# Performance work log

Hardware: AMD Instinct MI355X
Metric: run time of the kernel (lower is better)

The kernel has to match this reference:

```python
import jax, jax.numpy as jnp
import numpy as np

S, I, H, FC, O = 16384, 64, 1024, 128, 1


def setup_inputs() -> dict:
    key = jax.random.key(0)
    ks = jax.random.split(key, 9)
    s_lstm = 1.0 / np.sqrt(H)
    return {
        "input_seq": jax.random.normal(ks[0], (S, I), jnp.float32),
        "W_ih": jax.random.uniform(ks[1], (4 * H, I), jnp.float32, -s_lstm, s_lstm),
        "W_hh": jax.random.uniform(ks[2], (4 * H, H), jnp.float32, -s_lstm, s_lstm),
        "b_ih": jax.random.uniform(ks[3], (4 * H,), jnp.float32, -s_lstm, s_lstm),
        "b_hh": jax.random.uniform(ks[4], (4 * H,), jnp.float32, -s_lstm, s_lstm),
        "fc1_w": jax.random.uniform(ks[5], (FC, H), jnp.float32, -s_lstm, s_lstm),
        "fc1_b": jax.random.uniform(ks[6], (FC,), jnp.float32, -s_lstm, s_lstm),
        "fc2_w": jax.random.uniform(ks[7], (O, FC), jnp.float32, -1.0 / np.sqrt(FC), 1.0 / np.sqrt(FC)),
        "fc2_b": jax.random.uniform(ks[8], (O,), jnp.float32, -1.0 / np.sqrt(FC), 1.0 / np.sqrt(FC)),
    }


def _lstm_scan(x, W_ih, W_hh, b_ih, b_hh):
    # PyTorch gate order: i, f, g, o. batch=1 collapsed; x: [S, I]
    xg = x @ W_ih.T + (b_ih + b_hh)  # precompute input-side gates: [S, 4H]

    def step(carry, xg_t):
        h, c = carry
        gates = xg_t + h @ W_hh.T
        i, f, g, o = jnp.split(gates, 4)
        i = jax.nn.sigmoid(i)
        f = jax.nn.sigmoid(f)
        g = jnp.tanh(g)
        o = jax.nn.sigmoid(o)
        c = f * c + i * g
        h = o * jnp.tanh(c)
        return (h, c), h

    h0 = jnp.zeros((H,), x.dtype)
    c0 = jnp.zeros((H,), x.dtype)
    _, hs = jax.lax.scan(step, (h0, c0), xg)
    return hs  # [S, H]


def reference(input_seq, W_ih, W_hh, b_ih, b_hh, fc1_w, fc1_b, fc2_w, fc2_b):
    hs = _lstm_scan(input_seq, W_ih, W_hh, b_ih, b_hh)       # [S, H]
    x = jax.nn.relu(hs)                                       # relu on LSTM outputs
    x = jax.nn.relu(x @ fc1_w.T + fc1_b)                      # [S, 128]
    x = x @ fc2_w.T + fc2_b                                   # [S, 1]
    return x[-1]                                              # [1]
```

## Files before the change

kernel.cpp:

```cpp
#include <hip/hip_runtime.h>
#include <hip/hip_fp16.h>


#define S_LEN 16384
#define I_DIM 64
#define H_DIM 1024
#define NBLK  64
#define NTHR  512

typedef _Float16 half2_t __attribute__((ext_vector_type(2)));

__device__ __forceinline__ float sigmoidf_(float x) { return 1.0f / (1.0f + __expf(-x)); }
__device__ __forceinline__ float tanh_fast(float x) { return 1.0f - 2.0f / (__expf(2.0f * x) + 1.0f); }
__device__ __forceinline__ unsigned pack2(float a, float b) {
    return (unsigned)__half_as_ushort(__float2half(a)) |
           ((unsigned)__half_as_ushort(__float2half(b)) << 16);
}

__global__ __launch_bounds__(NTHR, 2) void lstm_persistent(
    const float* __restrict__ xseq,
    const float* __restrict__ W_ih,
    const float* __restrict__ W_hh,
    const float* __restrict__ b_ih,
    const float* __restrict__ b_hh,
    unsigned* __restrict__ pairs)
{
    const int b   = blockIdx.x;
    const int tid = threadIdx.x;
    const int w   = tid >> 6;
    const int c   = tid & 63;

    __shared__ unsigned h_stage[H_DIM / 2];
    __shared__ float    x_stage[2][I_DIM];
    __shared__ float    gs[64];
    __shared__ float    bias_s[64];

    unsigned wreg[8][8];
    float    wi[8];
    #pragma unroll
    for (int r = 0; r < 8; ++r) {
        const int rr   = 8 * w + r;
        const int grow = (rr >> 4) * H_DIM + 16 * b + (rr & 15);
        const float4* base = (const float4*)(W_hh + (size_t)grow * H_DIM);
        #pragma unroll
        for (int s = 0; s < 4; ++s) {
            const float4 f = base[s * 64 + c];
            wreg[r][2 * s]     = pack2(f.x, f.y);
            wreg[r][2 * s + 1] = pack2(f.z, f.w);
        }
        wi[r] = W_ih[(size_t)grow * I_DIM + c];
    }
    #pragma unroll
    for (int r = 0; r < 8; ++r)
        asm volatile("" : "+v"(wreg[r][0]), "+v"(wreg[r][1]), "+v"(wreg[r][2]),
                          "+v"(wreg[r][3]), "+v"(wreg[r][4]), "+v"(wreg[r][5]),
                          "+v"(wreg[r][6]), "+v"(wreg[r][7]));

    if (tid < 64) {
        const int grow = (tid >> 4) * H_DIM + 16 * b + (tid & 15);
        bias_s[tid] = b_ih[grow] + b_hh[grow];
    }
    float cst = 0.0f;
    h_stage[tid] = 0u;
    if (tid < 16) ((float4*)x_stage[0])[tid] = ((const float4*)xseq)[tid];
    __syncthreads();

    for (int t = 0; t < S_LEN; ++t) {
        if (w == 7 && c < 16 && t + 1 < S_LEN)
            ((float4*)x_stage[(t + 1) & 1])[c] =
                ((const float4*)(xseq + (size_t)(t + 1) * I_DIM))[c];

        float acc[8] = {0.f, 0.f, 0.f, 0.f, 0.f, 0.f, 0.f, 0.f};
        #pragma unroll
        for (int s = 0; s < 4; ++s) {
            const uint2 hv = *(const uint2*)&h_stage[s * 128 + 2 * c];
            const half2_t ha = __builtin_bit_cast(half2_t, hv.x);
            const half2_t hb = __builtin_bit_cast(half2_t, hv.y);
            #pragma unroll
            for (int r = 0; r < 8; ++r) {
                acc[r] = __builtin_amdgcn_fdot2(__builtin_bit_cast(half2_t, wreg[r][2 * s]),     ha, acc[r], false);
                acc[r] = __builtin_amdgcn_fdot2(__builtin_bit_cast(half2_t, wreg[r][2 * s + 1]), hb, acc[r], false);
            }
        }
        {
            const float xv = x_stage[t & 1][c];
            #pragma unroll
            for (int r = 0; r < 8; ++r) acc[r] = fmaf(wi[r], xv, acc[r]);
        }
        #pragma unroll
        for (int r = 0; r < 8; ++r) {
            #pragma unroll
            for (int off = 32; off > 0; off >>= 1)
                acc[r] += __shfl_xor(acc[r], off, 64);
        }
        if (c == 0) {
            #pragma unroll
            for (int r = 0; r < 8; ++r) gs[8 * w + r] = acc[r];
        }
        __syncthreads();

        if (tid < 16) {
            const float pi  = gs[tid]      + bias_s[tid];
            const float pfg = gs[16 + tid] + bias_s[16 + tid];
            const float pg  = gs[32 + tid] + bias_s[32 + tid];
            const float po  = gs[48 + tid] + bias_s[48 + tid];
            const float ig = sigmoidf_(pi);
            const float fg = sigmoidf_(pfg);
            const float gg = tanh_fast(pg);
            const float og = sigmoidf_(po);
            cst = fg * cst + ig * gg;
            const float h = og * tanh_fast(cst);
            const unsigned pk = ((unsigned)(t + 1) << 16) |
                                (unsigned)__half_as_ushort(__float2half(h));
            __hip_atomic_store(&pairs[(size_t)(t & 1) * H_DIM + 16 * b + tid], pk,
                               __ATOMIC_RELAXED, __HIP_MEMORY_SCOPE_AGENT);
        }

        if (t == S_LEN - 1) break;

        {
            const unsigned long long* P =
                (const unsigned long long*)(pairs + (size_t)(t & 1) * H_DIM);
            const unsigned long long tag  = (unsigned long long)(unsigned)(t + 1);
            const unsigned long long expv = (tag << 48) | (tag << 16);
            unsigned long long v;
            for (;;) {
                v = __hip_atomic_load(P + tid, __ATOMIC_RELAXED, __HIP_MEMORY_SCOPE_AGENT);
                if ((v & 0xFFFF0000FFFF0000ull) == expv) break;
                __builtin_amdgcn_s_sleep(1);
            }
            h_stage[tid] = (unsigned)(v & 0xFFFFu) | (((unsigned)(v >> 32) & 0xFFFFu) << 16);
        }
        __syncthreads();
    }
}

__global__ __launch_bounds__(256) void fc_head(
    const unsigned* __restrict__ pairs,
    const float* __restrict__ fc1_w,
    const float* __restrict__ fc1_b,
    const float* __restrict__ fc2_w,
    const float* __restrict__ fc2_b,
    float* __restrict__ out)
{
    const int tid = threadIdx.x;
    __shared__ float4 hr4[H_DIM / 4];
    __shared__ float  partial[256];
    __shared__ float  r1[128];

    const uint4 pa = ((const uint4*)(pairs + H_DIM))[tid];
    float4 hv = make_float4(__half2float(__ushort_as_half((unsigned short)(pa.x & 0xFFFFu))),
                            __half2float(__ushort_as_half((unsigned short)(pa.y & 0xFFFFu))),
                            __half2float(__ushort_as_half((unsigned short)(pa.z & 0xFFFFu))),
                            __half2float(__ushort_as_half((unsigned short)(pa.w & 0xFFFFu))));
    hv.x = fmaxf(hv.x, 0.f); hv.y = fmaxf(hv.y, 0.f);
    hv.z = fmaxf(hv.z, 0.f); hv.w = fmaxf(hv.w, 0.f);
    hr4[tid] = hv;
    __syncthreads();

    const int row = tid & 127, half = tid >> 7;
    const float4* wrow = (const float4*)(fc1_w + (size_t)row * H_DIM) + half * 128;
    float a0 = 0.f, a1 = 0.f;
    #pragma unroll 4
    for (int i = 0; i < 128; i += 2) {
        const float4 w0 = wrow[i],     h0 = hr4[half * 128 + i];
        const float4 w1 = wrow[i + 1], h1 = hr4[half * 128 + i + 1];
        a0 += w0.x * h0.x + w0.y * h0.y + w0.z * h0.z + w0.w * h0.w;
        a1 += w1.x * h1.x + w1.y * h1.y + w1.z * h1.z + w1.w * h1.w;
    }
    partial[tid] = a0 + a1;
    __syncthreads();
    if (tid < 128) {
        const float s = partial[tid] + partial[tid + 128] + fc1_b[tid];
        r1[tid] = fmaxf(s, 0.f);
    }
    __syncthreads();
    if (tid < 64) {
        float v = r1[tid] * fc2_w[tid] + r1[tid + 64] * fc2_w[tid + 64];
        #pragma unroll
        for (int off = 32; off > 0; off >>= 1) v += __shfl_xor(v, off, 64);
        if (tid == 0) out[0] = v + fc2_b[0];
    }
}

extern "C" void kernel_launch(void* const* d_in, const int* in_sizes, int n_in,
                              void* d_out, int out_size, void* d_ws, size_t ws_size,
                              hipStream_t stream) {
    (void)in_sizes; (void)n_in; (void)out_size; (void)ws_size;
    const float* xseq  = (const float*)d_in[0];
    const float* W_ih  = (const float*)d_in[1];
    const float* W_hh  = (const float*)d_in[2];
    const float* b_ih  = (const float*)d_in[3];
    const float* b_hh  = (const float*)d_in[4];
    const float* fc1_w = (const float*)d_in[5];
    const float* fc1_b = (const float*)d_in[6];
    const float* fc2_w = (const float*)d_in[7];
    const float* fc2_b = (const float*)d_in[8];
    unsigned* pairs = (unsigned*)d_ws;

    lstm_persistent<<<NBLK, NTHR, 0, stream>>>(xseq, W_ih, W_hh, b_ih, b_hh, pairs);
    fc_head<<<1, 256, 0, stream>>>(pairs, fc1_w, fc1_b, fc2_w, fc2_b, (float*)d_out);
}
```

Baseline: 41.11 ms.

## Fuse gate activations into each wave and exchange packed half2 hidden pairs

Each wave now owns two hidden units across all four gates. Lane 0 of the wave applies the activations right after the shuffle reduction, which removes the shared-memory gate staging and one block barrier per step. Hidden state is published as 64-bit words holding a 32-bit step tag and a packed half2 value. Each block writes its own results straight into a double-buffered shared h_stage and skips polling for them. The W_hh half2 registers are now reloaded from global memory every timestep before the spin-wait, which adds a large amount of per-step memory traffic.

```diff
diff --git a/kernel.cpp b/kernel.cpp
--- a/kernel.cpp
+++ b/kernel.cpp
@@ -16,6 +16,7 @@
     return (unsigned)__half_as_ushort(__float2half(a)) |
            ((unsigned)__half_as_ushort(__float2half(b)) << 16);
 }
+__device__ __forceinline__ half2_t as_h2(unsigned u) { return __builtin_bit_cast(half2_t, u); }
 
 __global__ __launch_bounds__(NTHR, 2) void lstm_persistent(
     const float* __restrict__ xseq,
@@ -23,63 +24,55 @@
     const float* __restrict__ W_hh,
     const float* __restrict__ b_ih,
     const float* __restrict__ b_hh,
-    unsigned* __restrict__ pairs)
+    unsigned long long* __restrict__ pairs)
 {
     const int b   = blockIdx.x;
     const int tid = threadIdx.x;
     const int w   = tid >> 6;
     const int c   = tid & 63;
 
-    __shared__ unsigned h_stage[H_DIM / 2];
+    __shared__ unsigned h_stage[2][H_DIM / 2];
     __shared__ float    x_stage[2][I_DIM];
-    __shared__ float    gs[64];
-    __shared__ float    bias_s[64];
-
-    unsigned wreg[8][8];
-    float    wi[8];
+
+    const float* wbase[8];
+    float wi[8], bias[8];
     #pragma unroll
     for (int r = 0; r < 8; ++r) {
-        const int rr   = 8 * w + r;
-        const int grow = (rr >> 4) * H_DIM + 16 * b + (rr & 15);
-        const float4* base = (const float4*)(W_hh + (size_t)grow * H_DIM);
+        const int grow = (r >> 1) * H_DIM + 16 * b + 2 * w + (r & 1);
+        wbase[r] = W_hh + (size_t)grow * H_DIM;
+        wi[r]    = W_ih[(size_t)grow * I_DIM + c];
+        bias[r]  = b_ih[grow] + b_hh[grow];
+    }
+    float cst0 = 0.f, cst1 = 0.f;
+
+    h_stage[0][tid] = 0u;
+    if (tid < 16) ((float4*)x_stage[0])[tid] = ((const float4*)xseq)[tid];
+    float4 xcur = make_float4(0.f, 0.f, 0.f, 0.f);
+    if (w == 7 && c < 16) xcur = ((const float4*)(xseq + (size_t)1 * I_DIM))[c];
+
+    unsigned wreg[8][8];
+    #pragma unroll
+    for (int r = 0; r < 8; ++r) {
+        const float4* b4 = (const float4*)wbase[r];
         #pragma unroll
         for (int s = 0; s < 4; ++s) {
-            const float4 f = base[s * 64 + c];
+            const float4 f = b4[s * 64 + c];
             wreg[r][2 * s]     = pack2(f.x, f.y);
             wreg[r][2 * s + 1] = pack2(f.z, f.w);
         }
-        wi[r] = W_ih[(size_t)grow * I_DIM + c];
-    }
-    #pragma unroll
-    for (int r = 0; r < 8; ++r)
-        asm volatile("" : "+v"(wreg[r][0]), "+v"(wreg[r][1]), "+v"(wreg[r][2]),
-                          "+v"(wreg[r][3]), "+v"(wreg[r][4]), "+v"(wreg[r][5]),
-                          "+v"(wreg[r][6]), "+v"(wreg[r][7]));
-
-    if (tid < 64) {
-        const int grow = (tid >> 4) * H_DIM + 16 * b + (tid & 15);
-        bias_s[tid] = b_ih[grow] + b_hh[grow];
-    }
-    float cst = 0.0f;
-    h_stage[tid] = 0u;
-    if (tid < 16) ((float4*)x_stage[0])[tid] = ((const float4*)xseq)[tid];
+    }
     __syncthreads();
 
     for (int t = 0; t < S_LEN; ++t) {
-        if (w == 7 && c < 16 && t + 1 < S_LEN)
-            ((float4*)x_stage[(t + 1) & 1])[c] =
-                ((const float4*)(xseq + (size_t)(t + 1) * I_DIM))[c];
-
         float acc[8] = {0.f, 0.f, 0.f, 0.f, 0.f, 0.f, 0.f, 0.f};
         #pragma unroll
         for (int s = 0; s < 4; ++s) {
-            const uint2 hv = *(const uint2*)&h_stage[s * 128 + 2 * c];
-            const half2_t ha = __builtin_bit_cast(half2_t, hv.x);
-            const half2_t hb = __builtin_bit_cast(half2_t, hv.y);
+            const uint2 hv = *(const uint2*)&h_stage[t & 1][s * 128 + 2 * c];
+            const half2_t ha = as_h2(hv.x), hb = as_h2(hv.y);
             #pragma unroll
             for (int r = 0; r < 8; ++r) {
-                acc[r] = __builtin_amdgcn_fdot2(__builtin_bit_cast(half2_t, wreg[r][2 * s]),     ha, acc[r], false);
-                acc[r] = __builtin_amdgcn_fdot2(__builtin_bit_cast(half2_t, wreg[r][2 * s + 1]), hb, acc[r], false);
+                acc[r] = __builtin_amdgcn_fdot2(as_h2(wreg[r][2 * s]),     ha, acc[r], false);
+                acc[r] = __builtin_amdgcn_fdot2(as_h2(wreg[r][2 * s + 1]), hb, acc[r], false);
             }
         }
         {
@@ -93,50 +86,69 @@
             for (int off = 32; off > 0; off >>= 1)
                 acc[r] += __shfl_xor(acc[r], off, 64);
         }
+
         if (c == 0) {
-            #pragma unroll
-            for (int r = 0; r < 8; ++r) gs[8 * w + r] = acc[r];
-        }
-        __syncthreads();
-
-        if (tid < 16) {
-            const float pi  = gs[tid]      + bias_s[tid];
-            const float pfg = gs[16 + tid] + bias_s[16 + tid];
-            const float pg  = gs[32 + tid] + bias_s[32 + tid];
-            const float po  = gs[48 + tid] + bias_s[48 + tid];
-            const float ig = sigmoidf_(pi);
-            const float fg = sigmoidf_(pfg);
-            const float gg = tanh_fast(pg);
-            const float og = sigmoidf_(po);
-            cst = fg * cst + ig * gg;
-            const float h = og * tanh_fast(cst);
-            const unsigned pk = ((unsigned)(t + 1) << 16) |
-                                (unsigned)__half_as_ushort(__float2half(h));
-            __hip_atomic_store(&pairs[(size_t)(t & 1) * H_DIM + 16 * b + tid], pk,
+            const float i0 = sigmoidf_(acc[0] + bias[0]);
+            const float f0 = sigmoidf_(acc[2] + bias[2]);
+            const float g0 = tanh_fast(acc[4] + bias[4]);
+            const float o0 = sigmoidf_(acc[6] + bias[6]);
+            cst0 = f0 * cst0 + i0 * g0;
+            const float h0 = o0 * tanh_fast(cst0);
+            const float i1 = sigmoidf_(acc[1] + bias[1]);
+            const float f1 = sigmoidf_(acc[3] + bias[3]);
+            const float g1 = tanh_fast(acc[5] + bias[5]);
+            const float o1 = sigmoidf_(acc[7] + bias[7]);
+            cst1 = f1 * cst1 + i1 * g1;
+            const float h1 = o1 * tanh_fast(cst1);
+            const unsigned lo = pack2(h0, h1);
+            const unsigned long long pk =
+                ((unsigned long long)(unsigned)(t + 1) << 32) | (unsigned long long)lo;
+            __hip_atomic_store(&pairs[(size_t)(t & 1) * (H_DIM / 2) + 8 * b + w], pk,
                                __ATOMIC_RELAXED, __HIP_MEMORY_SCOPE_AGENT);
+            h_stage[(t + 1) & 1][8 * b + w] = lo;
+        }
+
+        if (w == 7 && c < 16) {
+            if (t + 1 < S_LEN) ((float4*)x_stage[(t + 1) & 1])[c] = xcur;
+            const int tn = (t + 2 < S_LEN) ? t + 2 : S_LEN - 1;
+            xcur = ((const float4*)(xseq + (size_t)tn * I_DIM))[c];
         }
 
         if (t == S_LEN - 1) break;
 
-        {
-            const unsigned long long* P =
-                (const unsigned long long*)(pairs + (size_t)(t & 1) * H_DIM);
-            const unsigned long long tag  = (unsigned long long)(unsigned)(t + 1);
-            const unsigned long long expv = (tag << 48) | (tag << 16);
+        #pragma unroll
+        for (int r = 0; r < 8; ++r) {
+            const float4* b4 = (const float4*)wbase[r];
+            #pragma unroll
+            for (int s = 0; s < 4; ++s) {
+                const float4 f = b4[s * 64 + c];
+                wreg[r][2 * s]     = pack2(f.x, f.y);
+                wreg[r][2 * s + 1] = pack2(f.z, f.w);
+            }
+        }
+        #pragma unroll
+        for (int r = 0; r < 8; ++r)
+            asm volatile("" : "+v"(wreg[r][0]), "+v"(wreg[r][1]), "+v"(wreg[r][2]),
+                              "+v"(wreg[r][3]), "+v"(wreg[r][4]), "+v"(wreg[r][5]),
+                              "+v"(wreg[r][6]), "+v"(wreg[r][7]));
+
+        if ((tid >> 3) != b) {
+            const unsigned tag = (unsigned)(t + 1);
+            const unsigned long long* P = pairs + (size_t)(t & 1) * (H_DIM / 2);
             unsigned long long v;
             for (;;) {
                 v = __hip_atomic_load(P + tid, __ATOMIC_RELAXED, __HIP_MEMORY_SCOPE_AGENT);
-                if ((v & 0xFFFF0000FFFF0000ull) == expv) break;
+                if ((unsigned)(v >> 32) == tag) break;
                 __builtin_amdgcn_s_sleep(1);
             }
-            h_stage[tid] = (unsigned)(v & 0xFFFFu) | (((unsigned)(v >> 32) & 0xFFFFu) << 16);
+            h_stage[(t + 1) & 1][tid] = (unsigned)v;
         }
         __syncthreads();
     }
 }
 
 __global__ __launch_bounds__(256) void fc_head(
-    const unsigned* __restrict__ pairs,
+    const unsigned long long* __restrict__ pairs,
     const float* __restrict__ fc1_w,
     const float* __restrict__ fc1_b,
     const float* __restrict__ fc2_w,
@@ -148,11 +160,11 @@
     __shared__ float  partial[256];
     __shared__ float  r1[128];
 
-    const uint4 pa = ((const uint4*)(pairs + H_DIM))[tid];
+    const uint4 pa = ((const uint4*)pairs)[256 + tid];
     float4 hv = make_float4(__half2float(__ushort_as_half((unsigned short)(pa.x & 0xFFFFu))),
-                            __half2float(__ushort_as_half((unsigned short)(pa.y & 0xFFFFu))),
+                            __half2float(__ushort_as_half((unsigned short)(pa.x >> 16))),
                             __half2float(__ushort_as_half((unsigned short)(pa.z & 0xFFFFu))),
-                            __half2float(__ushort_as_half((unsigned short)(pa.w & 0xFFFFu))));
+                            __half2float(__ushort_as_half((unsigned short)(pa.z >> 16))));
     hv.x = fmaxf(hv.x, 0.f); hv.y = fmaxf(hv.y, 0.f);
     hv.z = fmaxf(hv.z, 0.f); hv.w = fmaxf(hv.w, 0.f);
     hr4[tid] = hv;
@@ -196,7 +208,7 @@
     const float* fc1_b = (const float*)d_in[6];
     const float* fc2_w = (const float*)d_in[7];
     const float* fc2_b = (const float*)d_in[8];
-    unsigned* pairs = (unsigned*)d_ws;
+    unsigned long long* pairs = (unsigned long long*)d_ws;
 
     lstm_persistent<<<NBLK, NTHR, 0, stream>>>(xseq, W_ih, W_hh, b_ih, b_hh, pairs);
     fc_head<<<1, 256, 0, stream>>>(pairs, fc1_w, fc1_b, fc2_w, fc2_b, (float*)d_out);
```

Result: slower. 56.35 ms (+37.1%).
